# Kernel tuning notes

Measured on AMD Instinct MI355X. Metric: run time of the kernel, lower is better.

## Reference

```python
import jax, jax.numpy as jnp
import numpy as np

DIM = 512
HEADS = 8
DIM_HEAD = 64
INNER = HEADS * DIM_HEAD


def setup_inputs() -> dict:
    key = jax.random.key(0)
    k1, k2, k3, k4 = jax.random.split(key, 4)
    x = jax.random.normal(k1, (4, 8192, DIM), dtype=jnp.float32)
    # nn.Linear(dim, inner*3, bias=False): weight applied as x @ W^T; store transposed form [dim, 3*inner]
    w_qkv = jax.random.normal(k2, (DIM, 3 * INNER), dtype=jnp.float32) / np.sqrt(DIM)
    w_out = jax.random.normal(k3, (INNER, DIM), dtype=jnp.float32) / np.sqrt(INNER)
    b_out = jax.random.normal(k4, (DIM,), dtype=jnp.float32) * 0.01
    return {"x": x, "w_qkv": w_qkv, "w_out": w_out, "b_out": b_out}


def reference(x, w_qkv, w_out, b_out):
    b, n, d = x.shape
    qkv = x @ w_qkv  # [b, n, 3*inner]
    q, k, v = jnp.split(qkv, 3, axis=-1)

    def to_heads(t):
        return t.reshape(b, n, HEADS, DIM_HEAD).transpose(0, 2, 1, 3)  # [b,h,n,dh]

    q, k, v = map(to_heads, (q, k, v))
    q = jax.nn.elu(q) + 1.0
    k = jax.nn.elu(k) + 1.0
    # kv summary: [b,h,dh,dh]
    kv = jnp.einsum('bhnd,bhnm->bhdm', k, v)
    # normalizer z: [b,h,n]  (note: original does NOT apply self.scale)
    z = 1.0 / (jnp.einsum('bhnd,bhd->bhn', q, k.sum(axis=2)) + 1e-6)
    out = jnp.einsum('bhnd,bhdm->bhnm', q, kv) * z[..., None]  # [b,h,n,dh]
    out = out.transpose(0, 2, 1, 3).reshape(b, n, INNER)
    return out @ w_out + b_out
```

## Files before the change

### kernel.cpp

```cpp
#include <hip/hip_runtime.h>
#include <hip/hip_bf16.h>

#define B_SZ 4
#define SEQ 8192
#define DIM 512
#define HEADS 8
#define DH 64
#define INNER 512
#define QKV_COLS 1536
#define M_TOT (B_SZ * SEQ)
#define BHN (B_SZ * HEADS)

typedef __bf16 bf16x8 __attribute__((ext_vector_type(8)));
typedef __bf16 bf16x4 __attribute__((ext_vector_type(4)));
typedef float f32x4 __attribute__((ext_vector_type(4)));

__device__ __forceinline__ float elu1(float x) {
    return x > 0.f ? x + 1.f : __expf(x);
}

__device__ __forceinline__ void gl_lds16(const void* g, void* l) {
    __builtin_amdgcn_global_load_lds(
        (const __attribute__((address_space(1))) unsigned int*)g,
        (__attribute__((address_space(3))) unsigned int*)l, 16, 0, 0);
}

#define MFMA16(a, b, c) __builtin_amdgcn_mfma_f32_16x16x32_bf16(a, b, c, 0, 0, 0)
#define BARRIER() asm volatile("s_barrier" ::: "memory")

__global__ void convert_all(const float* __restrict__ x,
                            const float* __restrict__ w_qkv,
                            const float* __restrict__ w_out,
                            __bf16* __restrict__ xb,
                            __bf16* __restrict__ wqkv_t,
                            __bf16* __restrict__ wout_t) {
    const int NX = M_TOT * DIM / 4;
    int id = blockIdx.x * 256 + threadIdx.x;
    if (id < NX) {
        float4 f = reinterpret_cast<const float4*>(x)[id];
        bf16x4 h = {(__bf16)f.x, (__bf16)f.y, (__bf16)f.z, (__bf16)f.w};
        reinterpret_cast<bf16x4*>(xb)[id] = h;
        return;
    }
    int id2 = id - NX;
    if (id2 < QKV_COLS * DIM) {
        int n = id2 / DIM, k = id2 % DIM;
        wqkv_t[id2] = (__bf16)w_qkv[k * QKV_COLS + n];
    } else {
        int id3 = id2 - QKV_COLS * DIM;
        if (id3 < INNER * DIM) {
            int n = id3 / DIM, k = id3 % DIM;
            wout_t[id3] = (__bf16)w_out[k * DIM + n];
        }
    }
}

__device__ __forceinline__ void gemm256_core(
    const __bf16* __restrict__ Am, const __bf16* __restrict__ Bm,
    int m0, int n0, char* smem, f32x4 acc[8][4])
{
    const int tid = threadIdx.x;
    const int wid = tid >> 6;
    const int lane = tid & 63;
    const int wm = wid >> 2, wn = wid & 3;
    const int lq = lane >> 4, lr = lane & 15;
    const int lrow = lane >> 3;
    const int lsw  = ((lane & 7) ^ lrow) * 8;

    __bf16* const As0 = (__bf16*)smem;
    __bf16* const Bs0 = (__bf16*)(smem + 32768);
    __bf16* const As1 = (__bf16*)(smem + 65536);
    __bf16* const Bs1 = (__bf16*)(smem + 98304);

    const int csw0 = ((0 + lq) ^ (lr & 7)) * 8;
    const int csw1 = ((4 + lq) ^ (lr & 7)) * 8;

    auto stageB = [&](__bf16* Bs, int kt, int u) {
        gl_lds16(&Bm[(size_t)(n0 + u * 64 + wid * 8 + lrow) * 512 + kt * 64 + lsw],
                 Bs + (u * 64 + wid * 8) * 64);
    };
    auto stageA = [&](__bf16* As, int kt, int s2) {
        int gr = (wid < 4) ? (s2 * 32 + wid * 8) : (128 + s2 * 32 + (wid - 4) * 8);
        gl_lds16(&Am[(size_t)(m0 + gr + lrow) * 512 + kt * 64 + lsw],
                 As + gr * 64);
    };
    auto ldA = [&](const __bf16* As, int m, int csw) -> bf16x8 {
        return *reinterpret_cast<const bf16x8*>(As + (wm * 128 + m * 16 + lr) * 64 + csw);
    };
    auto ldB = [&](const __bf16* Bs, int n, int csw) -> bf16x8 {
        return *reinterpret_cast<const bf16x8*>(Bs + (wn * 64 + n * 16 + lr) * 64 + csw);
    };

    stageB(Bs0, 0, 0); stageB(Bs0, 0, 1); stageB(Bs0, 0, 2); stageB(Bs0, 0, 3);
    stageA(As0, 0, 0); stageA(As0, 0, 1); stageA(As0, 0, 2); stageA(As0, 0, 3);
    asm volatile("s_waitcnt vmcnt(3)" ::: "memory");
    BARRIER();

#pragma unroll 2
    for (int t = 0; t < 8; ++t) {
        __bf16* const As  = (t & 1) ? As1 : As0;
        __bf16* const Bs  = (t & 1) ? Bs1 : Bs0;
        __bf16* const Asn = (t & 1) ? As0 : As1;
        __bf16* const Bsn = (t & 1) ? Bs0 : Bs1;
        const bool pf = (t < 7);
        bf16x8 bfr[4][2];

        {
            bf16x8 a00 = ldA(As, 0, csw0), a01 = ldA(As, 0, csw1);
            bf16x8 a10 = ldA(As, 1, csw0), a11 = ldA(As, 1, csw1);
#pragma unroll
            for (int n = 0; n < 4; ++n) { bfr[n][0] = ldB(Bs, n, csw0); bfr[n][1] = ldB(Bs, n, csw1); }
            if (pf) { stageB(Bsn, t + 1, 0); stageB(Bsn, t + 1, 1); }
            __builtin_amdgcn_s_setprio(1);
#pragma unroll
            for (int n = 0; n < 4; ++n) {
                acc[0][n] = MFMA16(a00, bfr[n][0], acc[0][n]);
                acc[0][n] = MFMA16(a01, bfr[n][1], acc[0][n]);
                acc[1][n] = MFMA16(a10, bfr[n][0], acc[1][n]);
                acc[1][n] = MFMA16(a11, bfr[n][1], acc[1][n]);
            }
            __builtin_amdgcn_s_setprio(0);
            if (pf) asm volatile("s_waitcnt vmcnt(4)" ::: "memory");
            else    asm volatile("s_waitcnt vmcnt(2)" ::: "memory");
            BARRIER();
        }
        {
            bf16x8 a00 = ldA(As, 2, csw0), a01 = ldA(As, 2, csw1);
            bf16x8 a10 = ldA(As, 3, csw0), a11 = ldA(As, 3, csw1);
            if (pf) { stageB(Bsn, t + 1, 2); stageB(Bsn, t + 1, 3); }
            __builtin_amdgcn_s_setprio(1);
#pragma unroll
            for (int n = 0; n < 4; ++n) {
                acc[2][n] = MFMA16(a00, bfr[n][0], acc[2][n]);
                acc[2][n] = MFMA16(a01, bfr[n][1], acc[2][n]);
                acc[3][n] = MFMA16(a10, bfr[n][0], acc[3][n]);
                acc[3][n] = MFMA16(a11, bfr[n][1], acc[3][n]);
            }
            __builtin_amdgcn_s_setprio(0);
            if (pf) asm volatile("s_waitcnt vmcnt(5)" ::: "memory");
            else    asm volatile("s_waitcnt vmcnt(1)" ::: "memory");
            BARRIER();
        }
        {
            bf16x8 a00 = ldA(As, 4, csw0), a01 = ldA(As, 4, csw1);
            bf16x8 a10 = ldA(As, 5, csw0), a11 = ldA(As, 5, csw1);
            if (pf) { stageA(Asn, t + 1, 0); stageA(Asn, t + 1, 1); }
            __builtin_amdgcn_s_setprio(1);
#pragma unroll
            for (int n = 0; n < 4; ++n) {
                acc[4][n] = MFMA16(a00, bfr[n][0], acc[4][n]);
                acc[4][n] = MFMA16(a01, bfr[n][1], acc[4][n]);
                acc[5][n] = MFMA16(a10, bfr[n][0], acc[5][n]);
                acc[5][n] = MFMA16(a11, bfr[n][1], acc[5][n]);
            }
            __builtin_amdgcn_s_setprio(0);
            if (pf) asm volatile("s_waitcnt vmcnt(6)" ::: "memory");
            else    asm volatile("s_waitcnt vmcnt(0)" ::: "memory");
            BARRIER();
        }
        {
            bf16x8 a00 = ldA(As, 6, csw0), a01 = ldA(As, 6, csw1);
            bf16x8 a10 = ldA(As, 7, csw0), a11 = ldA(As, 7, csw1);
            if (pf) { stageA(Asn, t + 1, 2); stageA(Asn, t + 1, 3); }
            __builtin_amdgcn_s_setprio(1);
#pragma unroll
            for (int n = 0; n < 4; ++n) {
                acc[6][n] = MFMA16(a00, bfr[n][0], acc[6][n]);
                acc[6][n] = MFMA16(a01, bfr[n][1], acc[6][n]);
                acc[7][n] = MFMA16(a10, bfr[n][0], acc[7][n]);
                acc[7][n] = MFMA16(a11, bfr[n][1], acc[7][n]);
            }
            __builtin_amdgcn_s_setprio(0);
            if (pf) asm volatile("s_waitcnt vmcnt(3)" ::: "memory");
            BARRIER();
        }
    }
}

#define TSTR 136
__launch_bounds__(512, 2)
__global__ void gemm_qkv(const __bf16* __restrict__ xb,
                         const __bf16* __restrict__ wqkv_t,
                         __bf16* __restrict__ q_ws,
                         __bf16* __restrict__ kT_ws,
                         __bf16* __restrict__ vT_ws) {
    __shared__ __attribute__((aligned(16))) char smem[131072];
    const int f  = blockIdx.y * gridDim.x + blockIdx.x;
    const int xc = f & 7, sl = f >> 3;
    const int m0 = (xc * 16 + sl / 6) * 256;
    const int n0 = (sl % 6) * 256;

    f32x4 acc[8][4] = {};
    gemm256_core(xb, wqkv_t, m0, n0, smem, acc);

    const int tid = threadIdx.x;
    const int wid = tid >> 6;
    const int lane = tid & 63;
    const int wm = wid >> 2, wn = wid & 3;
    const int lq = lane >> 4, lr = lane & 15;

    const int which = n0 / INNER;
    const int n0w = n0 % INNER;
    const int b = m0 / SEQ;
    const int nbase = m0 % SEQ;

    __bf16* const T0 = (__bf16*)smem;
    __bf16* const T1 = (__bf16*)(smem + 34816);

    if (which == 0) {
#pragma unroll
        for (int rh = 0; rh < 2; ++rh) {
            if (wm == rh) {
#pragma unroll
                for (int m = 0; m < 8; ++m)
#pragma unroll
                    for (int n = 0; n < 4; ++n) {
                        int col = wn * 64 + n * 16 + lr;
                        __bf16* Tb = (wn * 64 + n * 16 < 128) ? T0 : T1;
                        int cl = col & 127;
#pragma unroll
                        for (int r = 0; r < 4; ++r)
                            Tb[(m * 16 + lq * 4 + r) * TSTR + cl] =
                                (__bf16)elu1(acc[m][n][r]);
                    }
            }
            __syncthreads();
#pragma unroll
            for (int it = 0; it < 8; ++it) {
                int cch = tid + it * 512;
                int row = cch >> 5;
                int cc = (cch & 31) * 8;
                const __bf16* Tb = (cc < 128) ? T0 : T1;
                int dc = cc & 127;
                bf16x8 v = *reinterpret_cast<const bf16x8*>(&Tb[row * TSTR + dc]);
                int colg = n0w + cc;
                int h = colg >> 6, d = colg & 63;
                *reinterpret_cast<bf16x8*>(
                    &q_ws[(((size_t)(b * HEADS + h)) * SEQ + nbase + rh * 128 + row) * DH + d]) = v;
            }
            __syncthreads();
        }
    } else {
        __bf16* dst = (which == 1) ? kT_ws : vT_ws;
#pragma unroll
        for (int rh = 0; rh < 2; ++rh) {
            if (wm == rh) {
#pragma unroll
                for (int m = 0; m < 8; ++m) {
                    int rowb = m * 16 + lq * 4;
#pragma unroll
                    for (int n = 0; n < 4; ++n) {
                        int col = wn * 64 + n * 16 + lr;
                        __bf16* Tb = (wn * 64 + n * 16 < 128) ? T0 : T1;
                        int cl = col & 127;
                        bf16x4 h4;
#pragma unroll
                        for (int r = 0; r < 4; ++r) {
                            float v = acc[m][n][r];
                            h4[r] = (__bf16)((which == 1) ? elu1(v) : v);
                        }
                        *reinterpret_cast<bf16x4*>(&Tb[cl * TSTR + rowb]) = h4;
                    }
                }
            }
            __syncthreads();
#pragma unroll
            for (int it = 0; it < 8; ++it) {
                int cch = tid + it * 512;
                int colIdx = cch >> 4;
                int rc = (cch & 15) * 8;
                const __bf16* Tb = (colIdx < 128) ? T0 : T1;
                int cl = colIdx & 127;
                bf16x8 v = *reinterpret_cast<const bf16x8*>(&Tb[cl * TSTR + rc]);
                int g = n0w + colIdx;
                int h = g >> 6, d = g & 63;
                *reinterpret_cast<bf16x8*>(
                    &dst[(((size_t)(b * HEADS + h)) * DH + d) * SEQ + nbase + rh * 128 + rc]) = v;
            }
            __syncthreads();
        }
    }
}

__launch_bounds__(256, 2)
__global__ void kv_reduce(const __bf16* __restrict__ kT,
                          const __bf16* __restrict__ vT,
                          float* __restrict__ kv_t,
                          float* __restrict__ ksum) {
    __shared__ __attribute__((aligned(16))) __bf16 Ks[64][136];
    __shared__ __attribute__((aligned(16))) __bf16 Vs[64][136];
    const int tid = threadIdx.x;
    const int wid = tid >> 6;
    const int lane = tid & 63;
    const int lq = lane >> 4, lr = lane & 15;
    const int bh = blockIdx.y;
    const int n0 = blockIdx.x * 512;
    const size_t base = (size_t)bh * DH * SEQ;
    f32x4 acc[4] = {};
    f32x4 acc1 = {};
    bf16x8 ones8;
#pragma unroll
    for (int e = 0; e < 8; ++e) ones8[e] = (__bf16)1.f;

    for (int ch = 0; ch < 4; ++ch) {
        int nc = n0 + ch * 128;
#pragma unroll
        for (int t = 0; t < 4; ++t) {
            int c = tid + t * 256;
            int row = c >> 4, kc = (c & 15) * 8;
            *reinterpret_cast<bf16x8*>(&Ks[row][kc]) =
                *reinterpret_cast<const bf16x8*>(&kT[base + (size_t)row * SEQ + nc + kc]);
            *reinterpret_cast<bf16x8*>(&Vs[row][kc]) =
                *reinterpret_cast<const bf16x8*>(&vT[base + (size_t)row * SEQ + nc + kc]);
        }
        __syncthreads();
#pragma unroll
        for (int ks = 0; ks < 4; ++ks) {
            bf16x8 a = *reinterpret_cast<const bf16x8*>(&Ks[wid * 16 + lr][ks * 32 + lq * 8]);
            acc1 = MFMA16(a, ones8, acc1);
#pragma unroll
            for (int j = 0; j < 4; ++j) {
                bf16x8 b = *reinterpret_cast<const bf16x8*>(&Vs[j * 16 + lr][ks * 32 + lq * 8]);
                acc[j] = MFMA16(a, b, acc[j]);
            }
        }
        __syncthreads();
    }
    float* dst = kv_t + (size_t)bh * DH * DH;
#pragma unroll
    for (int j = 0; j < 4; ++j) {
        int m = j * 16 + lr;
#pragma unroll
        for (int r = 0; r < 4; ++r) {
            int d = wid * 16 + lq * 4 + r;
            atomicAdd(&dst[m * DH + d], acc[j][r]);
        }
    }
    if (lr == 0) {
#pragma unroll
        for (int r = 0; r < 4; ++r)
            atomicAdd(&ksum[bh * DH + wid * 16 + lq * 4 + r], acc1[r]);
    }
}

__launch_bounds__(256, 2)
__global__ void attn_kernel(const __bf16* __restrict__ q_ws,
                            const float* __restrict__ kv_t,
                            const float* __restrict__ ksum,
                            __bf16* __restrict__ attn) {
    __shared__ __attribute__((aligned(16))) __bf16 Qs[128][72];
    __shared__ __attribute__((aligned(16))) __bf16 KVs[64][72];
    __shared__ float zs[128];
    __shared__ float ks_s[64];
    const int tid = threadIdx.x;
    const int wid = tid >> 6, lane = tid & 63;
    const int lq = lane >> 4, lr = lane & 15;
    const int bh = blockIdx.y;
    const int b = bh >> 3, h = bh & 7;
    const int n0 = blockIdx.x * 128;
    const size_t qbase = ((size_t)bh * SEQ + n0) * DH;

#pragma unroll
    for (int t = 0; t < 4; ++t) {
        int c = tid + t * 256;
        int row = c >> 3, kc = (c & 7) * 8;
        *reinterpret_cast<bf16x8*>(&Qs[row][kc]) =
            *reinterpret_cast<const bf16x8*>(&q_ws[qbase + (size_t)row * DH + kc]);
    }
    const float* kvsrc = kv_t + (size_t)bh * DH * DH;
#pragma unroll
    for (int t = 0; t < 4; ++t) {
        int c = tid + t * 256;
        int m = c >> 4, dc = (c & 15) * 4;
        float4 f = *reinterpret_cast<const float4*>(&kvsrc[m * DH + dc]);
        bf16x4 h4 = {(__bf16)f.x, (__bf16)f.y, (__bf16)f.z, (__bf16)f.w};
        *reinterpret_cast<bf16x4*>(&KVs[m][dc]) = h4;
    }
    if (tid < 64) ks_s[tid] = ksum[bh * DH + tid];
    __syncthreads();
    {
        int row = tid >> 1, part = tid & 1;
        float s = 0.f;
#pragma unroll
        for (int j = 0; j < 32; ++j)
            s += (float)Qs[row][part * 32 + j] * ks_s[part * 32 + j];
        s += __shfl_xor(s, 1, 64);
        if (part == 0) zs[row] = 1.f / (s + 1e-6f);
    }
    __syncthreads();

    f32x4 acc[2][4] = {};
#pragma unroll
    for (int ks = 0; ks < 2; ++ks) {
        bf16x8 a0 = *reinterpret_cast<const bf16x8*>(&Qs[wid * 32 + lr][ks * 32 + lq * 8]);
        bf16x8 a1 = *reinterpret_cast<const bf16x8*>(&Qs[wid * 32 + 16 + lr][ks * 32 + lq * 8]);
#pragma unroll
        for (int j = 0; j < 4; ++j) {
            bf16x8 bfr = *reinterpret_cast<const bf16x8*>(&KVs[j * 16 + lr][ks * 32 + lq * 8]);
            acc[0][j] = MFMA16(a0, bfr, acc[0][j]);
            acc[1][j] = MFMA16(a1, bfr, acc[1][j]);
        }
    }
    __syncthreads();
#pragma unroll
    for (int mt = 0; mt < 2; ++mt)
#pragma unroll
        for (int j = 0; j < 4; ++j) {
            int m = j * 16 + lr;
#pragma unroll
            for (int r = 0; r < 4; ++r) {
                int row = wid * 32 + mt * 16 + lq * 4 + r;
                Qs[row][m] = (__bf16)(acc[mt][j][r] * zs[row]);
            }
        }
    __syncthreads();
#pragma unroll
    for (int it = 0; it < 4; ++it) {
        int c = tid + it * 256;
        int row = c >> 3, mc = (c & 7) * 8;
        bf16x8 v = *reinterpret_cast<const bf16x8*>(&Qs[row][mc]);
        *reinterpret_cast<bf16x8*>(
            &attn[((size_t)(b * SEQ + n0 + row)) * INNER + h * DH + mc]) = v;
    }
}

__launch_bounds__(512, 2)
__global__ void gemm_out(const __bf16* __restrict__ attn,
                         const __bf16* __restrict__ wout_t,
                         const float* __restrict__ b_out,
                         float* __restrict__ out) {
    __shared__ __attribute__((aligned(16))) char smem[131072];
    const int f  = blockIdx.y * gridDim.x + blockIdx.x;
    const int xc = f & 7, sl = f >> 3;
    const int m0 = (xc * 16 + (sl >> 1)) * 256;
    const int n0 = (sl & 1) * 256;

    f32x4 acc[8][4] = {};
    gemm256_core(attn, wout_t, m0, n0, smem, acc);

    const int tid = threadIdx.x;
    const int wid = tid >> 6;
    const int lane = tid & 63;
    const int wm = wid >> 2, wn = wid & 3;
    const int lq = lane >> 4, lr = lane & 15;

#pragma unroll
    for (int n = 0; n < 4; ++n) {
        int col = n0 + wn * 64 + n * 16 + lr;
        float bias = b_out[col];
#pragma unroll
        for (int m = 0; m < 8; ++m) {
            int row = m0 + wm * 128 + m * 16 + lq * 4;
#pragma unroll
            for (int r = 0; r < 4; ++r)
                out[(size_t)(row + r) * DIM + col] = acc[m][n][r] + bias;
        }
    }
}

extern "C" void kernel_launch(void* const* d_in, const int* in_sizes, int n_in,
                              void* d_out, int out_size, void* d_ws, size_t ws_size,
                              hipStream_t stream) {
    (void)in_sizes; (void)n_in; (void)out_size; (void)ws_size;
    const float* x     = (const float*)d_in[0];
    const float* w_qkv = (const float*)d_in[1];
    const float* w_out = (const float*)d_in[2];
    const float* b_out = (const float*)d_in[3];
    float* out = (float*)d_out;

    char* ws = (char*)d_ws;
    size_t off = 0;
    auto alloc = [&](size_t bytes) {
        char* p = ws + off;
        off += (bytes + 255) & ~(size_t)255;
        return p;
    };
    __bf16* xb     = (__bf16*)alloc((size_t)M_TOT * DIM * 2);
    __bf16* attn   = xb;
    __bf16* q_ws   = (__bf16*)alloc((size_t)BHN * SEQ * DH * 2);
    __bf16* kT_ws  = (__bf16*)alloc((size_t)BHN * SEQ * DH * 2);
    __bf16* vT_ws  = (__bf16*)alloc((size_t)BHN * SEQ * DH * 2);
    float*  kv_t   = (float*)alloc((size_t)BHN * DH * DH * 4 + (size_t)BHN * DH * 4);
    float*  ksum   = kv_t + (size_t)BHN * DH * DH;
    __bf16* wqkv_t = (__bf16*)alloc((size_t)QKV_COLS * DIM * 2);
    __bf16* wout_t = (__bf16*)alloc((size_t)INNER * DIM * 2);

    hipMemsetAsync(kv_t, 0, (size_t)BHN * DH * DH * 4 + (size_t)BHN * DH * 4, stream);
    convert_all<<<dim3(M_TOT * DIM / 4 / 256 + (QKV_COLS * DIM + INNER * DIM) / 256),
                  256, 0, stream>>>(x, w_qkv, w_out, xb, wqkv_t, wout_t);
    gemm_qkv<<<dim3(M_TOT / 256, QKV_COLS / 256), 512, 0, stream>>>(
        xb, wqkv_t, q_ws, kT_ws, vT_ws);
    kv_reduce<<<dim3(16, BHN), 256, 0, stream>>>(kT_ws, vT_ws, kv_t, ksum);
    attn_kernel<<<dim3(SEQ / 128, BHN), 256, 0, stream>>>(q_ws, kv_t, ksum, attn);
    gemm_out<<<dim3(M_TOT / 256, DIM / 256), 512, 0, stream>>>(attn, wout_t, b_out, out);
}
```

Measured before the change: 269.5 us.

## Replace pipelined 256x256 QKV GEMM with simple 128x128 single-buffered GEMM

The QKV projection kernel drops the shared, software-pipelined 256x256 GEMM core (512 threads, 128KB LDS, prefetch and setprio) and uses a simpler 128x128 tile with 256 threads, a single-buffered K loop, and a smaller LDS footprint. The epilogue is simplified to a single pass through a 128-row transpose buffer. The smaller LDS footprint and tile should raise occupancy and give more blocks for load balance. The cost is lower data reuse per tile and no overlap of global loads with MFMA work, since each K step waits on its own loads.

Measured after the change: 269.3 us. No clear change (-0.1%).

```diff
diff --git a/kernel.cpp b/kernel.cpp
--- a/kernel.cpp
+++ b/kernel.cpp
@@ -51,6 +51,117 @@
         if (id3 < INNER * DIM) {
             int n = id3 / DIM, k = id3 % DIM;
             wout_t[id3] = (__bf16)w_out[k * DIM + n];
+        }
+    }
+}
+
+#define TSTR 136
+__launch_bounds__(256, 2)
+__global__ void gemm_qkv(const __bf16* __restrict__ xb,
+                         const __bf16* __restrict__ wqkv_t,
+                         __bf16* __restrict__ q_ws,
+                         __bf16* __restrict__ kT_ws,
+                         __bf16* __restrict__ vT_ws) {
+    __shared__ __attribute__((aligned(16))) char smem[128 * TSTR * 2];
+    __bf16* As = (__bf16*)smem;
+    __bf16* Bs = (__bf16*)(smem + 16384);
+    __bf16* T  = (__bf16*)smem;
+
+    const int tid = threadIdx.x;
+    const int wid = tid >> 6;
+    const int lane = tid & 63;
+    const int wm = wid >> 1, wn = wid & 1;
+    const int lq = lane >> 4, lr = lane & 15;
+    const int m0 = blockIdx.x * 128;
+    const int n0 = blockIdx.y * 128;
+    const int lrow = lane >> 3;
+    const int lsw  = ((lane & 7) ^ lrow) * 8;
+
+    f32x4 acc[4][4] = {};
+
+    for (int kb = 0; kb < DIM; kb += 64) {
+#pragma unroll
+        for (int t = 0; t < 4; ++t) {
+            int qi = wid * 4 + t;
+            int row = qi * 8 + lrow;
+            gl_lds16(&xb[(size_t)(m0 + row) * DIM + kb + lsw], &As[qi * 512]);
+            gl_lds16(&wqkv_t[(size_t)(n0 + row) * DIM + kb + lsw], &Bs[qi * 512]);
+        }
+        __syncthreads();
+#pragma unroll
+        for (int ks = 0; ks < 2; ++ks) {
+            const int csw = ((ks * 4 + lq) ^ (lr & 7)) * 8;
+            bf16x8 af[4], bfv[4];
+#pragma unroll
+            for (int i = 0; i < 4; ++i)
+                af[i] = *reinterpret_cast<const bf16x8*>(
+                    &As[(wm * 64 + i * 16 + lr) * 64 + csw]);
+#pragma unroll
+            for (int j = 0; j < 4; ++j)
+                bfv[j] = *reinterpret_cast<const bf16x8*>(
+                    &Bs[(wn * 64 + j * 16 + lr) * 64 + csw]);
+#pragma unroll
+            for (int i = 0; i < 4; ++i)
+#pragma unroll
+                for (int j = 0; j < 4; ++j)
+                    acc[i][j] = MFMA16(af[i], bfv[j], acc[i][j]);
+        }
+        __syncthreads();
+    }
+
+    const int which = n0 / INNER;
+    const int n0w = n0 % INNER;
+    const int b = m0 / SEQ;
+    const int nbase = m0 % SEQ;
+
+    if (which == 0) {
+#pragma unroll
+        for (int i = 0; i < 4; ++i)
+#pragma unroll
+            for (int j = 0; j < 4; ++j) {
+                int col = wn * 64 + j * 16 + lr;
+#pragma unroll
+                for (int r = 0; r < 4; ++r)
+                    T[(wm * 64 + i * 16 + lq * 4 + r) * TSTR + col] =
+                        (__bf16)elu1(acc[i][j][r]);
+            }
+        __syncthreads();
+#pragma unroll
+        for (int it = 0; it < 8; ++it) {
+            int c = tid + it * 256;
+            int row = c >> 4, dc = (c & 15) * 8;
+            bf16x8 v = *reinterpret_cast<const bf16x8*>(&T[row * TSTR + dc]);
+            int col = n0w + dc;
+            int h = col >> 6, d = col & 63;
+            *reinterpret_cast<bf16x8*>(
+                &q_ws[(((size_t)(b * HEADS + h)) * SEQ + nbase + row) * DH + d]) = v;
+        }
+    } else {
+        __bf16* dst = (which == 1) ? kT_ws : vT_ws;
+#pragma unroll
+        for (int i = 0; i < 4; ++i)
+#pragma unroll
+            for (int j = 0; j < 4; ++j) {
+                int col = wn * 64 + j * 16 + lr;
+                int rowb = wm * 64 + i * 16 + lq * 4;
+                bf16x4 h4;
+#pragma unroll
+                for (int r = 0; r < 4; ++r) {
+                    float v = acc[i][j][r];
+                    h4[r] = (__bf16)((which == 1) ? elu1(v) : v);
+                }
+                *reinterpret_cast<bf16x4*>(&T[col * TSTR + rowb]) = h4;
+            }
+        __syncthreads();
+#pragma unroll
+        for (int it = 0; it < 8; ++it) {
+            int c = tid + it * 256;
+            int colIdx = c >> 4, rc = (c & 15) * 8;
+            bf16x8 v = *reinterpret_cast<const bf16x8*>(&T[colIdx * TSTR + rc]);
+            int gcol = n0w + colIdx;
+            int h = gcol >> 6, d = gcol & 63;
+            *reinterpret_cast<bf16x8*>(
+                &dst[(((size_t)(b * HEADS + h)) * DH + d) * SEQ + nbase + rc]) = v;
         }
     }
 }
@@ -173,111 +284,6 @@
             __builtin_amdgcn_s_setprio(0);
             if (pf) asm volatile("s_waitcnt vmcnt(3)" ::: "memory");
             BARRIER();
-        }
-    }
-}
-
-#define TSTR 136
-__launch_bounds__(512, 2)
-__global__ void gemm_qkv(const __bf16* __restrict__ xb,
-                         const __bf16* __restrict__ wqkv_t,
-                         __bf16* __restrict__ q_ws,
-                         __bf16* __restrict__ kT_ws,
-                         __bf16* __restrict__ vT_ws) {
-    __shared__ __attribute__((aligned(16))) char smem[131072];
-    const int f  = blockIdx.y * gridDim.x + blockIdx.x;
-    const int xc = f & 7, sl = f >> 3;
-    const int m0 = (xc * 16 + sl / 6) * 256;
-    const int n0 = (sl % 6) * 256;
-
-    f32x4 acc[8][4] = {};
-    gemm256_core(xb, wqkv_t, m0, n0, smem, acc);
-
-    const int tid = threadIdx.x;
-    const int wid = tid >> 6;
-    const int lane = tid & 63;
-    const int wm = wid >> 2, wn = wid & 3;
-    const int lq = lane >> 4, lr = lane & 15;
-
-    const int which = n0 / INNER;
-    const int n0w = n0 % INNER;
-    const int b = m0 / SEQ;
-    const int nbase = m0 % SEQ;
-
-    __bf16* const T0 = (__bf16*)smem;
-    __bf16* const T1 = (__bf16*)(smem + 34816);
-
-    if (which == 0) {
-#pragma unroll
-        for (int rh = 0; rh < 2; ++rh) {
-            if (wm == rh) {
-#pragma unroll
-                for (int m = 0; m < 8; ++m)
-#pragma unroll
-                    for (int n = 0; n < 4; ++n) {
-                        int col = wn * 64 + n * 16 + lr;
-                        __bf16* Tb = (wn * 64 + n * 16 < 128) ? T0 : T1;
-                        int cl = col & 127;
-#pragma unroll
-                        for (int r = 0; r < 4; ++r)
-                            Tb[(m * 16 + lq * 4 + r) * TSTR + cl] =
-                                (__bf16)elu1(acc[m][n][r]);
-                    }
-            }
-            __syncthreads();
-#pragma unroll
-            for (int it = 0; it < 8; ++it) {
-                int cch = tid + it * 512;
-                int row = cch >> 5;
-                int cc = (cch & 31) * 8;
-                const __bf16* Tb = (cc < 128) ? T0 : T1;
-                int dc = cc & 127;
-                bf16x8 v = *reinterpret_cast<const bf16x8*>(&Tb[row * TSTR + dc]);
-                int colg = n0w + cc;
-                int h = colg >> 6, d = colg & 63;
-                *reinterpret_cast<bf16x8*>(
-                    &q_ws[(((size_t)(b * HEADS + h)) * SEQ + nbase + rh * 128 + row) * DH + d]) = v;
-            }
-            __syncthreads();
-        }
-    } else {
-        __bf16* dst = (which == 1) ? kT_ws : vT_ws;
-#pragma unroll
-        for (int rh = 0; rh < 2; ++rh) {
-            if (wm == rh) {
-#pragma unroll
-                for (int m = 0; m < 8; ++m) {
-                    int rowb = m * 16 + lq * 4;
-#pragma unroll
-                    for (int n = 0; n < 4; ++n) {
-                        int col = wn * 64 + n * 16 + lr;
-                        __bf16* Tb = (wn * 64 + n * 16 < 128) ? T0 : T1;
-                        int cl = col & 127;
-                        bf16x4 h4;
-#pragma unroll
-                        for (int r = 0; r < 4; ++r) {
-                            float v = acc[m][n][r];
-                            h4[r] = (__bf16)((which == 1) ? elu1(v) : v);
-                        }
-                        *reinterpret_cast<bf16x4*>(&Tb[cl * TSTR + rowb]) = h4;
-                    }
-                }
-            }
-            __syncthreads();
-#pragma unroll
-            for (int it = 0; it < 8; ++it) {
-                int cch = tid + it * 512;
-                int colIdx = cch >> 4;
-                int rc = (cch & 15) * 8;
-                const __bf16* Tb = (colIdx < 128) ? T0 : T1;
-                int cl = colIdx & 127;
-                bf16x8 v = *reinterpret_cast<const bf16x8*>(&Tb[cl * TSTR + rc]);
-                int g = n0w + colIdx;
-                int h = g >> 6, d = g & 63;
-                *reinterpret_cast<bf16x8*>(
-                    &dst[(((size_t)(b * HEADS + h)) * DH + d) * SEQ + nbase + rh * 128 + rc]) = v;
-            }
-            __syncthreads();
         }
     }
 }
@@ -488,7 +494,7 @@
     hipMemsetAsync(kv_t, 0, (size_t)BHN * DH * DH * 4 + (size_t)BHN * DH * 4, stream);
     convert_all<<<dim3(M_TOT * DIM / 4 / 256 + (QKV_COLS * DIM + INNER * DIM) / 256),
                   256, 0, stream>>>(x, w_qkv, w_out, xb, wqkv_t, wout_t);
-    gemm_qkv<<<dim3(M_TOT / 256, QKV_COLS / 256), 512, 0, stream>>>(
+    gemm_qkv<<<dim3(M_TOT / 128, QKV_COLS / 128), 256, 0, stream>>>(
         xb, wqkv_t, q_ws, kT_ws, vT_ws);
     kv_reduce<<<dim3(16, BHN), 256, 0, stream>>>(kT_ws, vT_ws, kv_t, ksum);
     attn_kernel<<<dim3(SEQ / 128, BHN), 256, 0, stream>>>(q_ws, kv_t, ksum, attn);
```
